# Performance work log

Measured on AMD Instinct MI355X. Metric: run time of the kernel, lower is better.

The kernel has to match this reference:

```python
import jax, jax.numpy as jnp
import numpy as np

TOP_K = 2


def setup_inputs() -> dict:
    key = jax.random.key(0)
    k1, k2, k3, k4, k5 = jax.random.split(key, 5)
    B, S, D, E, F = 2, 1024, 2048, 8, 768
    scale_in = 1.0 / np.sqrt(D)
    scale_ff = 1.0 / np.sqrt(F)
    return {
        "x": jax.random.normal(k1, (B, S, D), dtype=jnp.float32),
        "w_gate_router": jax.random.normal(k2, (E, D), dtype=jnp.float32) * scale_in,
        "w_gate_proj": jax.random.normal(k3, (E, F, D), dtype=jnp.float32) * scale_in,
        "w_up_proj": jax.random.normal(k4, (E, F, D), dtype=jnp.float32) * scale_in,
        "w_down_proj": jax.random.normal(k5, (E, D, F), dtype=jnp.float32) * scale_ff,
    }


def moe_forward(x, w_gate_router, w_gate_proj, w_up_proj, w_down_proj):
    E = w_gate_router.shape[0]
    # Router: scores [B,S,E], top-k selection, softmax over the k selected scores.
    scores = jnp.einsum("bsd,ed->bse", x, w_gate_router)
    topk_scores, topk_idx = jax.lax.top_k(scores, TOP_K)          # [B,S,K]
    topk_probs = jax.nn.softmax(topk_scores, axis=-1)             # [B,S,K]
    # Dense combine weights: zero for unselected experts (== scatter of topk_probs).
    weights = jnp.sum(topk_probs[..., None] * jax.nn.one_hot(topk_idx, E, dtype=x.dtype), axis=-2)  # [B,S,E]
    # Per-expert SwiGLU computed densely over all tokens (same math as
    # gather/dispatch-per-expert followed by scatter-add combine).
    gate = jnp.einsum("bsd,efd->bsef", x, w_gate_proj)            # [B,S,E,F]
    up = jnp.einsum("bsd,efd->bsef", x, w_up_proj)
    hidden = jax.nn.silu(gate) * up                                # [B,S,E,F]
    # Weighted combine: sum_e weights[b,s,e] * (hidden @ w_down[e].T)
    out = jnp.einsum("bsef,edf,bse->bsd", hidden, w_down_proj, weights)
    return out


def reference(x, w_gate_router, w_gate_proj, w_up_proj, w_down_proj):
    return moe_forward(x, w_gate_router, w_gate_proj, w_up_proj, w_down_proj)
```

## Files before the change

kernel.cpp:

```cpp
#include <hip/hip_runtime.h>

#define T_TOK 2048
#define DIM   2048
#define NEXP  8
#define FF    768
#define NGRP  16

typedef unsigned short u16;
typedef unsigned int   u32;
typedef __bf16 bf16x8 __attribute__((ext_vector_type(8)));
typedef float  f32x4  __attribute__((ext_vector_type(4)));
typedef u16    u16x4  __attribute__((ext_vector_type(4)));
typedef u16    u16x8  __attribute__((ext_vector_type(8)));

#define AS1 __attribute__((address_space(1)))
#define AS3 __attribute__((address_space(3)))

__device__ __forceinline__ u16 f2bf(float f) {
    union { u32 i; float f; } v; v.f = f;
    u32 r = v.i + 0x7FFF + ((v.i >> 16) & 1);
    return (u16)(r >> 16);
}
__device__ __forceinline__ float bf2f(u16 u) {
    union { u32 i; float f; } v; v.i = ((u32)u) << 16; return v.f;
}

__device__ __forceinline__ void gload16(const u16* g, u16* l) {
    __builtin_amdgcn_global_load_lds((const AS1 u32*)g, (AS3 u32*)l, 16, 0, 0);
}

__global__ void cvt4_kernel(const float* __restrict__ s0, u16* __restrict__ d0, int n0,
                            const float* __restrict__ s1, u16* __restrict__ d1, int n1,
                            const float* __restrict__ s2, u16* __restrict__ d2, int n2,
                            const float* __restrict__ s3, u16* __restrict__ d3, int n3) {
    const float* s; u16* d; int n4;
    switch (blockIdx.y) {
        case 0: s = s0; d = d0; n4 = n0; break;
        case 1: s = s1; d = d1; n4 = n1; break;
        case 2: s = s2; d = d2; n4 = n2; break;
        default: s = s3; d = d3; n4 = n3; break;
    }
    int i = blockIdx.x * blockDim.x + threadIdx.x;
    int st = gridDim.x * blockDim.x;
    for (; i < n4; i += st) {
        f32x4 v = ((const f32x4*)s)[i];
        u16x4 o;
#pragma unroll
        for (int j = 0; j < 4; j++) o[j] = f2bf(v[j]);
        ((u16x4*)d)[i] = o;
    }
}

__global__ void router_kernel(const float* __restrict__ x, const float* __restrict__ wr,
                              int* cnt, int* rt_e, float* rt_p) {
    int t = blockIdx.x;
    int lane = threadIdx.x;
    float xv[32];
#pragma unroll
    for (int i = 0; i < 32; i++) xv[i] = x[(size_t)t * DIM + i * 64 + lane];
    float s[NEXP];
#pragma unroll
    for (int e = 0; e < NEXP; e++) {
        float acc = 0.f;
#pragma unroll
        for (int i = 0; i < 32; i++) acc += xv[i] * wr[(size_t)e * DIM + i * 64 + lane];
        for (int off = 32; off; off >>= 1) acc += __shfl_xor(acc, off);
        s[e] = acc;
    }
    if (lane == 0) {
        int bi = 0; float bv = s[0];
        for (int e = 1; e < NEXP; e++) if (s[e] > bv) { bv = s[e]; bi = e; }
        float sv = -1e30f; int si = 0;
        for (int e = 0; e < NEXP; e++) { if (e == bi) continue; if (s[e] > sv) { sv = s[e]; si = e; } }
        float p0 = 1.f / (1.f + __expf(sv - bv));
        float p1 = 1.f - p0;
        rt_e[t * 2 + 0] = bi; rt_e[t * 2 + 1] = si;
        rt_p[t * 2 + 0] = p0; rt_p[t * 2 + 1] = p1;
        atomicAdd(&cnt[bi * 2 + 0], 1);
        atomicAdd(&cnt[si * 2 + 1], 1);
    }
}

__global__ void scan_kernel(const int* cnt, int* base, int* tile_g, int* tile_m0, int* ntiles) {
    if (threadIdx.x == 0 && blockIdx.x == 0) {
        int off = 0, nt = 0;
        for (int g = 0; g < NGRP; g++) {
            base[g] = off;
            int c = cnt[g];
            for (int m0 = 0; m0 < c; m0 += 128) { tile_g[nt] = g; tile_m0[nt] = m0; nt++; }
            off += c;
        }
        *ntiles = nt;
    }
}

__global__ void assign_kernel(const int* rt_e, const float* rt_p, const int* base,
                              int* poscnt, int* rowtok, float* rowprob) {
    int t = blockIdx.x * blockDim.x + threadIdx.x;
    if (t >= T_TOK) return;
    for (int k = 0; k < 2; k++) {
        int g = rt_e[t * 2 + k] * 2 + k;
        int pos = atomicAdd(&poscnt[g], 1);
        int row = base[g] + pos;
        rowtok[row] = t;
        rowprob[row] = rt_p[t * 2 + k];
    }
}

__launch_bounds__(256)
__global__ void gateup_kernel(const u16* __restrict__ xb, const u16* __restrict__ wgb,
                              const u16* __restrict__ wub,
                              const int* cnt, const int* base, const int* tile_g,
                              const int* tile_m0, const int* ntiles,
                              const int* rowtok, const float* rowprob,
                              u16* __restrict__ hidden) {
    int tile = blockIdx.x;
    if (tile >= *ntiles) return;
    int g = tile_g[tile], m0 = tile_m0[tile];
    int e = g >> 1;
    int f0 = blockIdx.y * 64;
    int cg = cnt[g], bg_ = base[g];

    __shared__ u16 As[128 * 64];
    __shared__ u16 Bs[128 * 64];
    __shared__ int   tks[128];
    __shared__ float ps[128];

    int tid = threadIdx.x;
    if (tid < 128) {
        int valid = (m0 + tid) < cg;
        tks[tid] = valid ? rowtok[bg_ + m0 + tid] : 0;
        ps[tid]  = valid ? rowprob[bg_ + m0 + tid] : 0.f;
    }
    __syncthreads();

    int wave = tid >> 6, lane = tid & 63;
    int quad = lane >> 4, l16 = lane & 15;
    int wr = wave >> 1, wc = wave & 1;

    int r8   = lane >> 3;
    int koff = (lane & 7) * 8;
    const u16* ga[4]; const u16* gb[4];
    u16 *lA[4], *lB[4];
#pragma unroll
    for (int j = 0; j < 4; j++) {
        int arow = wave * 32 + j * 8 + r8;
        ga[j] = xb + (size_t)tks[arow] * DIM + koff;
        lA[j] = &As[(wave * 32 + j * 8) * 64];
        int c = wave * 2 + (j >> 1);
        const u16* src = (c & 1) ? wub : wgb;
        gb[j] = src + ((size_t)e * FF + f0 + (c >> 1) * 16 + (j & 1) * 8 + r8) * DIM + koff;
        lB[j] = &Bs[(wave * 32 + j * 8) * 64];
    }

    f32x4 acc[4][4] = {};

    for (int kk = 0; kk < DIM; kk += 64) {
#pragma unroll
        for (int j = 0; j < 4; j++) {
            gload16(ga[j] + kk, lA[j]);
            gload16(gb[j] + kk, lB[j]);
        }
        __syncthreads();
#pragma unroll
        for (int ks = 0; ks < 2; ks++) {
            bf16x8 a[4], b[4];
#pragma unroll
            for (int mi = 0; mi < 4; mi++)
                a[mi] = *(const bf16x8*)&As[(wr * 64 + mi * 16 + l16) * 64 + ks * 32 + quad * 8];
#pragma unroll
            for (int ni = 0; ni < 4; ni++)
                b[ni] = *(const bf16x8*)&Bs[(wc * 64 + ni * 16 + l16) * 64 + ks * 32 + quad * 8];
#pragma unroll
            for (int mi = 0; mi < 4; mi++)
#pragma unroll
                for (int ni = 0; ni < 4; ni++)
                    acc[mi][ni] = __builtin_amdgcn_mfma_f32_16x16x32_bf16(a[mi], b[ni], acc[mi][ni], 0, 0, 0);
        }
        __syncthreads();
    }

#pragma unroll
    for (int mi = 0; mi < 4; mi++) {
#pragma unroll
        for (int p = 0; p < 2; p++) {
            int f = f0 + (wc * 2 + p) * 16 + l16;
#pragma unroll
            for (int r = 0; r < 4; r++) {
                int m = wr * 64 + mi * 16 + quad * 4 + r;
                if (m0 + m < cg) {
                    float gv = acc[mi][p * 2][r], uv = acc[mi][p * 2 + 1][r];
                    float h = (gv / (1.f + __expf(-gv))) * uv * ps[m];
                    hidden[(size_t)(bg_ + m0 + m) * FF + f] = f2bf(h);
                }
            }
        }
    }
}

__launch_bounds__(256)
__global__ void down_kernel(const u16* __restrict__ hid, const u16* __restrict__ wdb,
                            const int* cnt, const int* base, const int* tile_g,
                            const int* tile_m0, const int* ntiles, const int* rowtok,
                            u16* __restrict__ out0, u16* __restrict__ out1) {
    int tile = blockIdx.x;
    if (tile >= *ntiles) return;
    int g = tile_g[tile], m0 = tile_m0[tile];
    int e = g >> 1, slot = g & 1;
    int d0 = blockIdx.y * 128;
    int cg = cnt[g], bg_ = base[g];

    __shared__ u16 As[128 * 64];
    __shared__ u16 Bs[128 * 64];
    __shared__ int tks[128];

    int tid = threadIdx.x;
    if (tid < 128) tks[tid] = ((m0 + tid) < cg) ? rowtok[bg_ + m0 + tid] : 0;
    __syncthreads();

    int wave = tid >> 6, lane = tid & 63;
    int quad = lane >> 4, l16 = lane & 15;
    int wr = wave >> 1, wc = wave & 1;

    int r8   = lane >> 3;
    int koff = (lane & 7) * 8;
    const u16* ga[4]; const u16* gb[4];
    u16 *lA[4], *lB[4];
#pragma unroll
    for (int j = 0; j < 4; j++) {
        ga[j] = hid + (size_t)(bg_ + m0 + wave * 32 + j * 8 + r8) * FF + koff;
        lA[j] = &As[(wave * 32 + j * 8) * 64];
        gb[j] = wdb + ((size_t)e * DIM + d0 + wave * 32 + j * 8 + r8) * FF + koff;
        lB[j] = &Bs[(wave * 32 + j * 8) * 64];
    }

    f32x4 acc[4][4] = {};

    for (int kk = 0; kk < FF; kk += 64) {
#pragma unroll
        for (int j = 0; j < 4; j++) {
            gload16(ga[j] + kk, lA[j]);
            gload16(gb[j] + kk, lB[j]);
        }
        __syncthreads();
#pragma unroll
        for (int ks = 0; ks < 2; ks++) {
            bf16x8 a[4], b[4];
#pragma unroll
            for (int mi = 0; mi < 4; mi++)
                a[mi] = *(const bf16x8*)&As[(wr * 64 + mi * 16 + l16) * 64 + ks * 32 + quad * 8];
#pragma unroll
            for (int ni = 0; ni < 4; ni++)
                b[ni] = *(const bf16x8*)&Bs[(wc * 64 + ni * 16 + l16) * 64 + ks * 32 + quad * 8];
#pragma unroll
            for (int mi = 0; mi < 4; mi++)
#pragma unroll
                for (int ni = 0; ni < 4; ni++)
                    acc[mi][ni] = __builtin_amdgcn_mfma_f32_16x16x32_bf16(a[mi], b[ni], acc[mi][ni], 0, 0, 0);
        }
        __syncthreads();
    }

    u16* outp = slot ? out1 : out0;
#pragma unroll
    for (int mi = 0; mi < 4; mi++) {
#pragma unroll
        for (int ni = 0; ni < 4; ni++) {
            int d = d0 + wc * 64 + ni * 16 + l16;
#pragma unroll
            for (int r = 0; r < 4; r++) {
                int m = wr * 64 + mi * 16 + quad * 4 + r;
                if (m0 + m < cg) {
                    outp[(size_t)tks[m] * DIM + d] = f2bf(acc[mi][ni][r]);
                }
            }
        }
    }
}

__global__ void combine_kernel(const u16* __restrict__ o0, const u16* __restrict__ o1,
                               float* __restrict__ out) {
    int i = blockIdx.x * blockDim.x + threadIdx.x;
    u16x8 a = *(const u16x8*)(o0 + (size_t)i * 8);
    u16x8 b = *(const u16x8*)(o1 + (size_t)i * 8);
    f32x4 r0, r1;
#pragma unroll
    for (int j = 0; j < 4; j++) {
        r0[j] = bf2f(a[j]) + bf2f(b[j]);
        r1[j] = bf2f(a[4 + j]) + bf2f(b[4 + j]);
    }
    *(f32x4*)(out + (size_t)i * 8) = r0;
    *(f32x4*)(out + (size_t)i * 8 + 4) = r1;
}

extern "C" void kernel_launch(void* const* d_in, const int* in_sizes, int n_in,
                              void* d_out, int out_size, void* d_ws, size_t ws_size,
                              hipStream_t stream) {
    const float* x  = (const float*)d_in[0];
    const float* wr = (const float*)d_in[1];
    const float* wg = (const float*)d_in[2];
    const float* wu = (const float*)d_in[3];
    const float* wd = (const float*)d_in[4];
    float* out = (float*)d_out;

    char* W = (char*)d_ws;
    int*   cnt     = (int*)(W + 0);
    int*   poscnt  = (int*)(W + 64);
    int*   base    = (int*)(W + 128);
    int*   ntiles  = (int*)(W + 192);
    int*   tile_g  = (int*)(W + 256);
    int*   tile_m0 = (int*)(W + 512);
    int*   rt_e    = (int*)(W + 1024);
    float* rt_p    = (float*)(W + 20480);
    int*   rowtok  = (int*)(W + 40960);
    float* rowprob = (float*)(W + 61440);
    u16*   hidden  = (u16*)(W + 81920);
    u16*   xb      = (u16*)(W + ((size_t)8  << 20));
    u16*   wgb     = (u16*)(W + ((size_t)17 << 20));
    u16*   wub     = (u16*)(W + ((size_t)43 << 20));
    u16*   wdb     = (u16*)(W + ((size_t)69 << 20));
    u16*   out0    = (u16*)(W + ((size_t)17 << 20));
    u16*   out1    = (u16*)(W + ((size_t)26 << 20));

    hipMemsetAsync(W, 0, 256, stream);

    const int NW = NEXP * FF * DIM / 4;
    const int NX = T_TOK * DIM / 4;
    cvt4_kernel<<<dim3(1536, 4), 256, 0, stream>>>(x, xb, NX, wg, wgb, NW, wu, wub, NW, wd, wdb, NW);

    router_kernel<<<T_TOK, 64, 0, stream>>>(x, wr, cnt, rt_e, rt_p);
    scan_kernel<<<1, 64, 0, stream>>>(cnt, base, tile_g, tile_m0, ntiles);
    assign_kernel<<<8, 256, 0, stream>>>(rt_e, rt_p, base, poscnt, rowtok, rowprob);

    gateup_kernel<<<dim3(48, 12), 256, 0, stream>>>(xb, wgb, wub, cnt, base, tile_g, tile_m0,
                                                    ntiles, rowtok, rowprob, hidden);
    down_kernel<<<dim3(48, 16), 256, 0, stream>>>(hidden, wdb, cnt, base, tile_g, tile_m0,
                                                  ntiles, rowtok, out0, out1);
    combine_kernel<<<T_TOK * DIM / (256 * 8), 256, 0, stream>>>(out0, out1, out);
}
```

Before: 412.4 us.

## Replace direct-to-LDS loads with register-prefetched double-stage pipeline in MoE GEMMs

Both the gate/up and down GEMM kernels stop using global_load_lds and halve the K tile to 32. They now prefetch the next K slice into registers while MFMAs run on the current slice held in shared memory. The goal is to overlap global memory latency with matrix compute, since the old loop serialized load, barrier and compute. The cost is extra VGPR pressure, twice as many loop iterations with two barriers each, and a narrower LDS row stride that may change bank-conflict behaviour.

```diff
diff --git a/kernel.cpp b/kernel.cpp
--- a/kernel.cpp
+++ b/kernel.cpp
@@ -13,9 +13,6 @@
 typedef u16    u16x4  __attribute__((ext_vector_type(4)));
 typedef u16    u16x8  __attribute__((ext_vector_type(8)));
 
-#define AS1 __attribute__((address_space(1)))
-#define AS3 __attribute__((address_space(3)))
-
 __device__ __forceinline__ u16 f2bf(float f) {
     union { u32 i; float f; } v; v.f = f;
     u32 r = v.i + 0x7FFF + ((v.i >> 16) & 1);
@@ -23,10 +20,6 @@
 }
 __device__ __forceinline__ float bf2f(u16 u) {
     union { u32 i; float f; } v; v.i = ((u32)u) << 16; return v.f;
-}
-
-__device__ __forceinline__ void gload16(const u16* g, u16* l) {
-    __builtin_amdgcn_global_load_lds((const AS1 u32*)g, (AS3 u32*)l, 16, 0, 0);
 }
 
 __global__ void cvt4_kernel(const float* __restrict__ s0, u16* __restrict__ d0, int n0,
@@ -121,8 +114,8 @@
     int f0 = blockIdx.y * 64;
     int cg = cnt[g], bg_ = base[g];
 
-    __shared__ u16 As[128 * 64];
-    __shared__ u16 Bs[128 * 64];
+    __shared__ u16 As[128 * 32];
+    __shared__ u16 Bs[128 * 32];
     __shared__ int   tks[128];
     __shared__ float ps[128];
 
@@ -138,46 +131,45 @@
     int quad = lane >> 4, l16 = lane & 15;
     int wr = wave >> 1, wc = wave & 1;
 
-    int r8   = lane >> 3;
-    int koff = (lane & 7) * 8;
-    const u16* ga[4]; const u16* gb[4];
-    u16 *lA[4], *lB[4];
-#pragma unroll
-    for (int j = 0; j < 4; j++) {
-        int arow = wave * 32 + j * 8 + r8;
-        ga[j] = xb + (size_t)tks[arow] * DIM + koff;
-        lA[j] = &As[(wave * 32 + j * 8) * 64];
-        int c = wave * 2 + (j >> 1);
-        const u16* src = (c & 1) ? wub : wgb;
-        gb[j] = src + ((size_t)e * FF + f0 + (c >> 1) * 16 + (j & 1) * 8 + r8) * DIM + koff;
-        lB[j] = &Bs[(wave * 32 + j * 8) * 64];
-    }
+    int r4   = lane >> 2;
+    int koff = (lane & 3) * 8;
+    const u16* ga0 = xb + (size_t)tks[wave * 32 + r4] * DIM + koff;
+    const u16* ga1 = xb + (size_t)tks[wave * 32 + 16 + r4] * DIM + koff;
+    const u16* gb0 = wgb + ((size_t)e * FF + f0 + wave * 16 + r4) * DIM + koff;
+    const u16* gb1 = wub + ((size_t)e * FF + f0 + wave * 16 + r4) * DIM + koff;
+    u16* uA0 = &As[(wave * 32 + r4) * 32 + koff];
+    u16* uA1 = &As[(wave * 32 + 16 + r4) * 32 + koff];
+    u16* uB0 = &Bs[(wave * 32 + r4) * 32 + koff];
+    u16* uB1 = &Bs[(wave * 32 + 16 + r4) * 32 + koff];
 
     f32x4 acc[4][4] = {};
 
-    for (int kk = 0; kk < DIM; kk += 64) {
-#pragma unroll
-        for (int j = 0; j < 4; j++) {
-            gload16(ga[j] + kk, lA[j]);
-            gload16(gb[j] + kk, lB[j]);
-        }
+    u16x8 pa0 = *(const u16x8*)ga0, pa1 = *(const u16x8*)ga1;
+    u16x8 pb0 = *(const u16x8*)gb0, pb1 = *(const u16x8*)gb1;
+
+    for (int kk = 0; kk < DIM; kk += 32) {
         __syncthreads();
-#pragma unroll
-        for (int ks = 0; ks < 2; ks++) {
-            bf16x8 a[4], b[4];
-#pragma unroll
-            for (int mi = 0; mi < 4; mi++)
-                a[mi] = *(const bf16x8*)&As[(wr * 64 + mi * 16 + l16) * 64 + ks * 32 + quad * 8];
+        *(u16x8*)uA0 = pa0; *(u16x8*)uA1 = pa1;
+        *(u16x8*)uB0 = pb0; *(u16x8*)uB1 = pb1;
+        __syncthreads();
+        if (kk + 32 < DIM) {
+            pa0 = *(const u16x8*)(ga0 + kk + 32);
+            pa1 = *(const u16x8*)(ga1 + kk + 32);
+            pb0 = *(const u16x8*)(gb0 + kk + 32);
+            pb1 = *(const u16x8*)(gb1 + kk + 32);
+        }
+        bf16x8 a[4], b[4];
+#pragma unroll
+        for (int mi = 0; mi < 4; mi++)
+            a[mi] = *(const bf16x8*)&As[(wr * 64 + mi * 16 + l16) * 32 + quad * 8];
+#pragma unroll
+        for (int ni = 0; ni < 4; ni++)
+            b[ni] = *(const bf16x8*)&Bs[(wc * 64 + ni * 16 + l16) * 32 + quad * 8];
+#pragma unroll
+        for (int mi = 0; mi < 4; mi++)
 #pragma unroll
             for (int ni = 0; ni < 4; ni++)
-                b[ni] = *(const bf16x8*)&Bs[(wc * 64 + ni * 16 + l16) * 64 + ks * 32 + quad * 8];
-#pragma unroll
-            for (int mi = 0; mi < 4; mi++)
-#pragma unroll
-                for (int ni = 0; ni < 4; ni++)
-                    acc[mi][ni] = __builtin_amdgcn_mfma_f32_16x16x32_bf16(a[mi], b[ni], acc[mi][ni], 0, 0, 0);
-        }
-        __syncthreads();
+                acc[mi][ni] = __builtin_amdgcn_mfma_f32_16x16x32_bf16(a[mi], b[ni], acc[mi][ni], 0, 0, 0);
     }
 
 #pragma unroll
@@ -210,8 +202,8 @@
     int d0 = blockIdx.y * 128;
     int cg = cnt[g], bg_ = base[g];
 
-    __shared__ u16 As[128 * 64];
-    __shared__ u16 Bs[128 * 64];
+    __shared__ u16 As[128 * 32];
+    __shared__ u16 Bs[128 * 32];
     __shared__ int tks[128];
 
     int tid = threadIdx.x;
@@ -222,43 +214,45 @@
     int quad = lane >> 4, l16 = lane & 15;
     int wr = wave >> 1, wc = wave & 1;
 
-    int r8   = lane >> 3;
-    int koff = (lane & 7) * 8;
-    const u16* ga[4]; const u16* gb[4];
-    u16 *lA[4], *lB[4];
-#pragma unroll
-    for (int j = 0; j < 4; j++) {
-        ga[j] = hid + (size_t)(bg_ + m0 + wave * 32 + j * 8 + r8) * FF + koff;
-        lA[j] = &As[(wave * 32 + j * 8) * 64];
-        gb[j] = wdb + ((size_t)e * DIM + d0 + wave * 32 + j * 8 + r8) * FF + koff;
-        lB[j] = &Bs[(wave * 32 + j * 8) * 64];
-    }
+    int r4   = lane >> 2;
+    int koff = (lane & 3) * 8;
+    const u16* ga0 = hid + (size_t)(bg_ + m0 + wave * 32 + r4) * FF + koff;
+    const u16* ga1 = hid + (size_t)(bg_ + m0 + wave * 32 + 16 + r4) * FF + koff;
+    const u16* gb0 = wdb + ((size_t)e * DIM + d0 + wave * 32 + r4) * FF + koff;
+    const u16* gb1 = wdb + ((size_t)e * DIM + d0 + wave * 32 + 16 + r4) * FF + koff;
+    u16* uA0 = &As[(wave * 32 + r4) * 32 + koff];
+    u16* uA1 = &As[(wave * 32 + 16 + r4) * 32 + koff];
+    u16* uB0 = &Bs[(wave * 32 + r4) * 32 + koff];
+    u16* uB1 = &Bs[(wave * 32 + 16 + r4) * 32 + koff];
 
     f32x4 acc[4][4] = {};
 
-    for (int kk = 0; kk < FF; kk += 64) {
-#pragma unroll
-        for (int j = 0; j < 4; j++) {
-            gload16(ga[j] + kk, lA[j]);
-            gload16(gb[j] + kk, lB[j]);
-        }
+    u16x8 pa0 = *(const u16x8*)ga0, pa1 = *(const u16x8*)ga1;
+    u16x8 pb0 = *(const u16x8*)gb0, pb1 = *(const u16x8*)gb1;
+
+    for (int kk = 0; kk < FF; kk += 32) {
         __syncthreads();
-#pragma unroll
-        for (int ks = 0; ks < 2; ks++) {
-            bf16x8 a[4], b[4];
-#pragma unroll
-            for (int mi = 0; mi < 4; mi++)
-                a[mi] = *(const bf16x8*)&As[(wr * 64 + mi * 16 + l16) * 64 + ks * 32 + quad * 8];
+        *(u16x8*)uA0 = pa0; *(u16x8*)uA1 = pa1;
+        *(u16x8*)uB0 = pb0; *(u16x8*)uB1 = pb1;
+        __syncthreads();
+        if (kk + 32 < FF) {
+            pa0 = *(const u16x8*)(ga0 + kk + 32);
+            pa1 = *(const u16x8*)(ga1 + kk + 32);
+            pb0 = *(const u16x8*)(gb0 + kk + 32);
+            pb1 = *(const u16x8*)(gb1 + kk + 32);
+        }
+        bf16x8 a[4], b[4];
+#pragma unroll
+        for (int mi = 0; mi < 4; mi++)
+            a[mi] = *(const bf16x8*)&As[(wr * 64 + mi * 16 + l16) * 32 + quad * 8];
+#pragma unroll
+        for (int ni = 0; ni < 4; ni++)
+            b[ni] = *(const bf16x8*)&Bs[(wc * 64 + ni * 16 + l16) * 32 + quad * 8];
+#pragma unroll
+        for (int mi = 0; mi < 4; mi++)
 #pragma unroll
             for (int ni = 0; ni < 4; ni++)
-                b[ni] = *(const bf16x8*)&Bs[(wc * 64 + ni * 16 + l16) * 64 + ks * 32 + quad * 8];
-#pragma unroll
-            for (int mi = 0; mi < 4; mi++)
-#pragma unroll
-                for (int ni = 0; ni < 4; ni++)
-                    acc[mi][ni] = __builtin_amdgcn_mfma_f32_16x16x32_bf16(a[mi], b[ni], acc[mi][ni], 0, 0, 0);
-        }
-        __syncthreads();
+                acc[mi][ni] = __builtin_amdgcn_mfma_f32_16x16x32_bf16(a[mi], b[ni], acc[mi][ni], 0, 0, 0);
     }
 
     u16* outp = slot ? out1 : out0;
```

Result: faster. 392.3 us (-4.9%).
